# Optimization experiments

Hardware: AMD Instinct MI355X
Metric: run time of the kernel (lower is better)

## Reference

```python
import jax, jax.numpy as jnp
import numpy as np
from jax import lax

K = 3  # kernel_size
PAD = 1
STRIDE = 1
DIL = 1


def setup_inputs() -> dict:
    key = jax.random.key(0)
    k1, k2 = jax.random.split(key)
    x = jax.random.normal(k1, (32, 256, 56, 56), dtype=jnp.float32)
    weights = jax.random.normal(k2, (256, 256, K * K), dtype=jnp.float32) * 0.05
    return {"x": x, "weights": weights}


def reference(x, weights):
    B, C, H, W = x.shape
    O = weights.shape[0]
    # weights stored as [O, C, k*k] -> standard OIHW conv kernel
    w = weights.reshape(O, C, K, K)
    # Dense conv replaces the per-(channel, filter) matmul loop over im2col windows.
    y = lax.conv_general_dilated(
        x, w,
        window_strides=(STRIDE, STRIDE),
        padding=[(PAD, PAD), (PAD, PAD)],
        rhs_dilation=(DIL, DIL),
        dimension_numbers=("NCHW", "OIHW", "NCHW"),
    )  # [B, O, Hout, Wout]
    Hout, Wout = y.shape[2], y.shape[3]
    # Faithful to original: results buffer is laid out [O, B, Hout, Wout]
    # (out-channel-major blocks of batch) then reinterpreted as [B, O, Hout, Wout].
    result = jnp.transpose(y, (1, 0, 2, 3)).reshape(B, O, Hout, Wout)
    return result
```

## Files before the change

kernel.cpp:

```cpp
#include <hip/hip_runtime.h>
#include <hip/hip_bf16.h>

using s8v   = __attribute__((ext_vector_type(8))) short;
using f32x4 = __attribute__((ext_vector_type(4))) float;

#define N_TOT 100352
#define WT_ELEMS 589824
#define PLANE_ELEMS 861184
#define XT_ELEMS 27557888
#define WS_NEED  56295424

#define BAR() asm volatile("s_barrier" ::: "memory")

__device__ __forceinline__ unsigned short f2bf(float f) {
    unsigned int u = __float_as_uint(f);
    unsigned int r = (u + 0x7FFF + ((u >> 16) & 1)) >> 16;
    return (unsigned short)r;
}

__device__ __forceinline__ void gl_lds16(const void* g, void* l) {
    __builtin_amdgcn_global_load_lds(
        (const __attribute__((address_space(1))) unsigned int*)g,
        (__attribute__((address_space(3))) unsigned int*)l, 16, 0, 0);
}

__global__ void prep_w(const float* __restrict__ w, unsigned short* __restrict__ wt) {
    int u = blockIdx.x * 256 + threadIdx.x;
    int kt = u >> 11;
    int r  = u & 2047;
    int o  = r >> 3;
    int s  = r & 7;
    int ksub  = s ^ (o & 7);
    int kstep = kt * 2 + (ksub >> 2);
    int cb = kstep / 9, tap = kstep - cb * 9;
    int c0 = cb * 32 + (ksub & 3) * 8;
    const float* src = w + ((size_t)(o * 256 + c0)) * 9 + tap;
    unsigned int p[4];
    #pragma unroll
    for (int q = 0; q < 4; ++q) {
        float f0 = src[(2 * q) * 9];
        float f1 = src[(2 * q + 1) * 9];
        p[q] = (unsigned)f2bf(f0) | ((unsigned)f2bf(f1) << 16);
    }
    *(uint4*)(wt + (size_t)u * 8) = *(uint4*)p;
}

__global__ void prep_x(const float* __restrict__ x, unsigned short* __restrict__ xt) {
    int b  = blockIdx.x / 58;
    int hp = blockIdx.x % 58;
    int tid = threadIdx.x;
    uint4 zero = {0u, 0u, 0u, 0u};
    size_t rowbase = (size_t)(b * 58 + hp) * 58;
    if (hp == 0 || hp == 57) {
        for (int i = tid; i < 1856; i += 256) {
            int cg = i / 58, wp = i - cg * 58;
            *(uint4*)(xt + ((size_t)cg * PLANE_ELEMS + (rowbase + wp) * 8)) = zero;
        }
        return;
    }
    int h = hp - 1;
    int wave = tid >> 6, lane = tid & 63;
    for (int cg = wave; cg < 32; cg += 4) {
        unsigned short* outp = xt + (size_t)cg * PLANE_ELEMS + rowbase * 8;
        if (lane < 56) {
            const float* src = x + ((size_t)(b * 256 + cg * 8) * 3136 + h * 56 + lane);
            unsigned int p[4];
            #pragma unroll
            for (int q = 0; q < 4; ++q) {
                float f0 = src[(size_t)(2 * q) * 3136];
                float f1 = src[(size_t)(2 * q + 1) * 3136];
                p[q] = (unsigned)f2bf(f0) | ((unsigned)f2bf(f1) << 16);
            }
            *(uint4*)(outp + (size_t)(lane + 1) * 8) = *(uint4*)p;
        } else if (lane == 56) {
            *(uint4*)outp = zero;
        } else if (lane == 57) {
            *(uint4*)(outp + 57 * 8) = zero;
        }
    }
}

__global__ __launch_bounds__(512, 2) void gemm8(const unsigned short* __restrict__ wt,
                                                const unsigned short* __restrict__ xt,
                                                float* __restrict__ out) {
    extern __shared__ char lds[];
    int bx = blockIdx.x;
    int nt = (bx & 7) * 49 + (bx >> 3);
    int tid  = threadIdx.x;
    int w    = tid >> 6, lane = tid & 63;
    int l16  = lane & 15, quad = lane >> 4;
    int wm   = w >> 2,   wn   = w & 3;
    int lane16 = lane * 16;

    int s0 = w * 2, s1 = w * 2 + 1;
    int adst0 = ((s0 >> 3) * 128 + (s0 & 7) * 8) * 128;
    int adst1 = ((s1 >> 3) * 128 + (s1 & 7) * 8) * 128;
    int bp0 = ((s0 >> 2) * 64 + (s0 & 3) * 8);
    int bp1 = ((s1 >> 2) * 64 + (s1 & 3) * 8);
    int bdst0 = bp0 * 128;
    int bdst1 = bp1 * 128;
    int ksub  = (lane & 7) ^ (lane >> 3);
    int ksl   = ksub >> 2;
    int c2off = (ksub & 3) * PLANE_ELEMS;
    int pix[2][2];
    #pragma unroll
    for (int it = 0; it < 2; ++it)
        #pragma unroll
        for (int h = 0; h < 2; ++h) {
            int n = nt * 256 + (it ? bp1 : bp0) + h * 32 + (lane >> 3);
            int b = n / 3136; int rr = n - b * 3136;
            int hh = rr / 56; int ww = rr - hh * 56;
            pix[it][h] = ((b * 58 + hh) * 58 + ww) * 8;
        }
    int pix00 = pix[0][0], pix01 = pix[0][1], pix10 = pix[1][0], pix11 = pix[1][1];

    int swz = (quad ^ (l16 & 7)) << 4;
    int aK0 = wm * 16384 + l16 * 128 + swz;
    int aK1 = aK0 ^ 64;
    int bK0 = 32768 + wn * 8192 + l16 * 128 + swz;
    int bK1 = bK0 ^ 64;

    auto SA = [&](char* buf, const char* srcTile, int roff) {
        gl_lds16(srcTile + adst0 + roff + lane16, buf + adst0 + roff);
        gl_lds16(srcTile + adst1 + roff + lane16, buf + adst1 + roff);
    };
    auto SB = [&](char* buf, int bo0, int bo1, int h) {
        int bsel = (ksl ? bo1 : bo0) + c2off;
        gl_lds16(xt + (size_t)(unsigned)(bsel + (h ? pix01 : pix00)),
                 buf + 32768 + bdst0 + h * 4096);
        gl_lds16(xt + (size_t)(unsigned)(bsel + (h ? pix11 : pix10)),
                 buf + 32768 + bdst1 + h * 4096);
    };
    auto BO = [&](int ks) {
        int cb = ks / 9, tap = ks - cb * 9;
        return cb * 4 * PLANE_ELEMS + ((tap / 3) * 58 + (tap - (tap / 3) * 3)) * 8;
    };

    f32x4 acc[8][4] = {};
    s8v a0[4], a1[4], b00[2], b01[2], b10[2], b11[2];

    SA(lds, (const char*)wt, 0);
    SA(lds, (const char*)wt, 8192);
    SB(lds, BO(0), BO(1), 0);
    SB(lds, BO(0), BO(1), 1);
    SA(lds + 65536, (const char*)wt + 32768, 0);
    SB(lds + 65536, BO(2), BO(3), 0);
    SB(lds + 65536, BO(2), BO(3), 1);
    asm volatile("s_waitcnt vmcnt(6)" ::: "memory");
    BAR();

    #define PHASE_MFMA(MH, NH, BA, BB)                                             \
        __builtin_amdgcn_s_setprio(1);                                             \
        _Pragma("unroll")                                                          \
        for (int f = 0; f < 4; ++f) {                                              \
            _Pragma("unroll")                                                      \
            for (int g = 0; g < 2; ++g) {                                          \
                f32x4 c = acc[(MH)*4 + f][(NH)*2 + g];                             \
                c = __builtin_amdgcn_mfma_f32_16x16x32_bf16(a0[f], BA[g], c, 0, 0, 0); \
                c = __builtin_amdgcn_mfma_f32_16x16x32_bf16(a1[f], BB[g], c, 0, 0, 0); \
                acc[(MH)*4 + f][(NH)*2 + g] = c;                                   \
            }                                                                      \
        }                                                                          \
        __builtin_amdgcn_s_setprio(0);

    #pragma unroll 1
    for (int t = 0; t < 36; ++t) {
        char* bufc = lds + (t & 1) * 65536;
        char* bufo = lds + ((t & 1) ^ 1) * 65536;
        const char* wA1 = (const char*)wt + (size_t)(t + 1) * 32768;
        const char* wA0 = (const char*)wt + (size_t)(t + 2) * 32768;
        int kk  = 2 * (t + 2);
        int bo0 = BO(kk);
        int bo1 = BO(kk + 1);

        #pragma unroll
        for (int f = 0; f < 4; ++f) {
            a0[f] = *(const s8v*)(bufc + aK0 + f * 2048);
            a1[f] = *(const s8v*)(bufc + aK1 + f * 2048);
        }
        #pragma unroll
        for (int g = 0; g < 2; ++g) {
            b00[g] = *(const s8v*)(bufc + bK0 + g * 2048);
            b01[g] = *(const s8v*)(bufc + bK1 + g * 2048);
        }
        if (t < 35) SA(bufo, wA1, 8192);
        BAR();
        PHASE_MFMA(0, 0, b00, b01)
        BAR();

        #pragma unroll
        for (int g = 0; g < 2; ++g) {
            b10[g] = *(const s8v*)(bufc + bK0 + 4096 + g * 2048);
            b11[g] = *(const s8v*)(bufc + bK1 + 4096 + g * 2048);
        }
        if (t < 34) SA(bufc, wA0, 0);
        BAR();
        PHASE_MFMA(0, 1, b10, b11)
        BAR();

        #pragma unroll
        for (int f = 0; f < 4; ++f) {
            a0[f] = *(const s8v*)(bufc + aK0 + 8192 + f * 2048);
            a1[f] = *(const s8v*)(bufc + aK1 + 8192 + f * 2048);
        }
        if (t < 34) SB(bufc, bo0, bo1, 0);
        BAR();
        PHASE_MFMA(1, 0, b00, b01)
        BAR();

        if (t < 34) {
            SB(bufc, bo0, bo1, 1);
            asm volatile("s_waitcnt vmcnt(6)" ::: "memory");
        } else if (t == 34) {
            asm volatile("s_waitcnt vmcnt(0)" ::: "memory");
        }
        BAR();
        PHASE_MFMA(1, 1, b10, b11)
        BAR();
    }

    float* op = out + (size_t)(wm * 128 + quad * 4) * N_TOT + nt * 256 + wn * 64 + l16;
    #pragma unroll
    for (int f = 0; f < 8; ++f)
        #pragma unroll
        for (int rr = 0; rr < 4; ++rr) {
            float* orow = op + (size_t)(f * 16 + rr) * N_TOT;
            #pragma unroll
            for (int g = 0; g < 4; ++g)
                orow[g * 16] = acc[f][g][rr];
        }
}

__global__ void conv_naive(const float* __restrict__ x, const float* __restrict__ wq,
                           float* __restrict__ out) {
    int f = blockIdx.x * 256 + threadIdx.x;
    int o = f / N_TOT;
    int n = f - o * N_TOT;
    int b = n / 3136; int r = n - b * 3136; int h = r / 56; int w = r - h * 56;
    const float* xb = x + (size_t)b * 256 * 3136;
    const float* wo = wq + o * 2304;
    float acc = 0.f;
    for (int c = 0; c < 256; ++c) {
        const float* xc = xb + c * 3136;
        const float* wc = wo + c * 9;
        #pragma unroll
        for (int dh = 0; dh < 3; ++dh) {
            int ih = h + dh - 1;
            if (ih < 0 || ih >= 56) continue;
            const float* xr = xc + ih * 56;
            #pragma unroll
            for (int dw = 0; dw < 3; ++dw) {
                int iw = w + dw - 1;
                if (iw >= 0 && iw < 56) acc += xr[iw] * wc[dh * 3 + dw];
            }
        }
    }
    out[f] = acc;
}

extern "C" void kernel_launch(void* const* d_in, const int* in_sizes, int n_in,
                              void* d_out, int out_size, void* d_ws, size_t ws_size,
                              hipStream_t stream) {
    const float* x = (const float*)d_in[0];
    const float* w = (const float*)d_in[1];
    float* out = (float*)d_out;
    if (ws_size >= (size_t)WS_NEED) {
        unsigned short* wt = (unsigned short*)d_ws;
        unsigned short* xt = wt + WT_ELEMS;
        static int attr_done = 0;
        if (!attr_done) {
            hipFuncSetAttribute((const void*)gemm8,
                                hipFuncAttributeMaxDynamicSharedMemorySize, 131072);
            attr_done = 1;
        }
        prep_w<<<288, 256, 0, stream>>>(w, wt);
        prep_x<<<32 * 58, 256, 0, stream>>>(x, xt);
        gemm8<<<392, 512, 131072, stream>>>(wt, xt, out);
    } else {
        conv_naive<<<N_TOT, 256, 0, stream>>>(x, w, out);
    }
}
```

Measured before the change: 328.7 us.

## Double-buffer register fragments and cut barriers in conv GEMM main loop

Splits the A/B register fragments into even and odd sets so the next quarter's LDS reads, and the next tile's first-quarter reads from the other buffer, are issued before the current MFMA batch runs. This drops from two barriers per phase to one. MFMA ordering changes from interleaved K0/K1 pairs to two separate passes, and the vmcnt gating becomes a per-phase macro. It raises register pressure and relies on subtle LDS hazard ordering, since the other buffer is read while asynchronous global-to-LDS loads are still in flight.

Result: faster. 321.2 us (-2.3%).

```diff
diff --git a/kernel.cpp b/kernel.cpp
--- a/kernel.cpp
+++ b/kernel.cpp
@@ -11,6 +11,8 @@
 #define WS_NEED  56295424
 
 #define BAR() asm volatile("s_barrier" ::: "memory")
+#define GATE(T) do { if ((T) < 33) asm volatile("s_waitcnt vmcnt(8)" ::: "memory"); \
+                     else          asm volatile("s_waitcnt vmcnt(0)" ::: "memory"); } while (0)
 
 __device__ __forceinline__ unsigned short f2bf(float f) {
     unsigned int u = __float_as_uint(f);
@@ -137,7 +139,26 @@
     };
 
     f32x4 acc[8][4] = {};
-    s8v a0[4], a1[4], b00[2], b01[2], b10[2], b11[2];
+    s8v aE0[4], aE1[4], aO0[4], aO1[4];
+    s8v bE0[2], bE1[2], bO0[2], bO1[2];
+
+    #define MFMA_Q(MH, NH, A0, A1, B0, B1)                                         \
+        __builtin_amdgcn_s_setprio(1);                                             \
+        _Pragma("unroll")                                                          \
+        for (int f = 0; f < 4; ++f) {                                              \
+            _Pragma("unroll")                                                      \
+            for (int g = 0; g < 2; ++g)                                            \
+                acc[(MH)*4+f][(NH)*2+g] = __builtin_amdgcn_mfma_f32_16x16x32_bf16( \
+                    A0[f], B0[g], acc[(MH)*4+f][(NH)*2+g], 0, 0, 0);               \
+        }                                                                          \
+        _Pragma("unroll")                                                          \
+        for (int f = 0; f < 4; ++f) {                                              \
+            _Pragma("unroll")                                                      \
+            for (int g = 0; g < 2; ++g)                                            \
+                acc[(MH)*4+f][(NH)*2+g] = __builtin_amdgcn_mfma_f32_16x16x32_bf16( \
+                    A1[f], B1[g], acc[(MH)*4+f][(NH)*2+g], 0, 0, 0);               \
+        }                                                                          \
+        __builtin_amdgcn_s_setprio(0);
 
     SA(lds, (const char*)wt, 0);
     SA(lds, (const char*)wt, 8192);
@@ -148,20 +169,16 @@
     SB(lds + 65536, BO(2), BO(3), 1);
     asm volatile("s_waitcnt vmcnt(6)" ::: "memory");
     BAR();
-
-    #define PHASE_MFMA(MH, NH, BA, BB)                                             \
-        __builtin_amdgcn_s_setprio(1);                                             \
-        _Pragma("unroll")                                                          \
-        for (int f = 0; f < 4; ++f) {                                              \
-            _Pragma("unroll")                                                      \
-            for (int g = 0; g < 2; ++g) {                                          \
-                f32x4 c = acc[(MH)*4 + f][(NH)*2 + g];                             \
-                c = __builtin_amdgcn_mfma_f32_16x16x32_bf16(a0[f], BA[g], c, 0, 0, 0); \
-                c = __builtin_amdgcn_mfma_f32_16x16x32_bf16(a1[f], BB[g], c, 0, 0, 0); \
-                acc[(MH)*4 + f][(NH)*2 + g] = c;                                   \
-            }                                                                      \
-        }                                                                          \
-        __builtin_amdgcn_s_setprio(0);
+    #pragma unroll
+    for (int f = 0; f < 4; ++f) {
+        aE0[f] = *(const s8v*)(lds + aK0 + f * 2048);
+        aE1[f] = *(const s8v*)(lds + aK1 + f * 2048);
+    }
+    #pragma unroll
+    for (int g = 0; g < 2; ++g) {
+        bE0[g] = *(const s8v*)(lds + bK0 + g * 2048);
+        bE1[g] = *(const s8v*)(lds + bK1 + g * 2048);
+    }
 
     #pragma unroll 1
     for (int t = 0; t < 36; ++t) {
@@ -173,50 +190,51 @@
         int bo0 = BO(kk);
         int bo1 = BO(kk + 1);
 
-        #pragma unroll
-        for (int f = 0; f < 4; ++f) {
-            a0[f] = *(const s8v*)(bufc + aK0 + f * 2048);
-            a1[f] = *(const s8v*)(bufc + aK1 + f * 2048);
-        }
+        BAR();
         #pragma unroll
         for (int g = 0; g < 2; ++g) {
-            b00[g] = *(const s8v*)(bufc + bK0 + g * 2048);
-            b01[g] = *(const s8v*)(bufc + bK1 + g * 2048);
+            bO0[g] = *(const s8v*)(bufc + bK0 + 4096 + g * 2048);
+            bO1[g] = *(const s8v*)(bufc + bK1 + 4096 + g * 2048);
         }
         if (t < 35) SA(bufo, wA1, 8192);
+        MFMA_Q(0, 0, aE0, aE1, bE0, bE1)
+        GATE(t);
+
         BAR();
-        PHASE_MFMA(0, 0, b00, b01)
+        #pragma unroll
+        for (int f = 0; f < 4; ++f)
+            aO0[f] = *(const s8v*)(bufc + aK0 + 8192 + f * 2048);
+        if (t < 34) SA(bufc, wA0, 0);
+        MFMA_Q(0, 1, aE0, aE1, bO0, bO1)
+        GATE(t);
+
         BAR();
-
-        #pragma unroll
-        for (int g = 0; g < 2; ++g) {
-            b10[g] = *(const s8v*)(bufc + bK0 + 4096 + g * 2048);
-            b11[g] = *(const s8v*)(bufc + bK1 + 4096 + g * 2048);
-        }
-        if (t < 34) SA(bufc, wA0, 0);
+        #pragma unroll
+        for (int f = 0; f < 4; ++f)
+            aO1[f] = *(const s8v*)(bufc + aK1 + 8192 + f * 2048);
+        if (t < 35) {
+            #pragma unroll
+            for (int f = 0; f < 4; ++f)
+                aE0[f] = *(const s8v*)(bufo + aK0 + f * 2048);
+        }
+        if (t < 34) SB(bufc, bo0, bo1, 0);
+        MFMA_Q(1, 0, aO0, aO1, bE0, bE1)
+        GATE(t);
+
         BAR();
-        PHASE_MFMA(0, 1, b10, b11)
-        BAR();
-
-        #pragma unroll
-        for (int f = 0; f < 4; ++f) {
-            a0[f] = *(const s8v*)(bufc + aK0 + 8192 + f * 2048);
-            a1[f] = *(const s8v*)(bufc + aK1 + 8192 + f * 2048);
-        }
-        if (t < 34) SB(bufc, bo0, bo1, 0);
-        BAR();
-        PHASE_MFMA(1, 0, b00, b01)
-        BAR();
-
-        if (t < 34) {
-            SB(bufc, bo0, bo1, 1);
-            asm volatile("s_waitcnt vmcnt(6)" ::: "memory");
-        } else if (t == 34) {
-            asm volatile("s_waitcnt vmcnt(0)" ::: "memory");
-        }
-        BAR();
-        PHASE_MFMA(1, 1, b10, b11)
-        BAR();
+        if (t < 35) {
+            #pragma unroll
+            for (int f = 0; f < 4; ++f)
+                aE1[f] = *(const s8v*)(bufo + aK1 + f * 2048);
+            #pragma unroll
+            for (int g = 0; g < 2; ++g) {
+                bE0[g] = *(const s8v*)(bufo + bK0 + g * 2048);
+                bE1[g] = *(const s8v*)(bufo + bK1 + g * 2048);
+            }
+        }
+        if (t < 34) SB(bufc, bo0, bo1, 1);
+        MFMA_Q(1, 1, aO0, aO1, bO0, bO1)
+        GATE(t);
     }
 
     float* op = out + (size_t)(wm * 128 + quad * 4) * N_TOT + nt * 256 + wn * 64 + l16;
```
